# Optimization experiments

Hardware: AMD Instinct MI355X
Metric: run time of the kernel (lower is better)

## Reference

```python
import jax, jax.numpy as jnp
import numpy as np

B, S, D = 1, 2048, 128   # batch, seq_len, num_hidden (== head dim)
H, KVH = 32, 8           # num_heads, num_kv_heads
REP = H // KVH           # num_rep = 4
D_K = 128                # softmax scale denominator sqrt(d_k)
ROPE_THETA = 10000.0


def _rope(x):
    # x: (B, h, S, D). Standard rotate-half RoPE over last dim, positions on axis -2.
    inv_freq = 1.0 / (ROPE_THETA ** (jnp.arange(0, D, 2, dtype=jnp.float32) / D))  # (D/2,)
    ang = jnp.arange(S, dtype=jnp.float32)[:, None] * inv_freq                      # (S, D/2)
    cos = jnp.concatenate([jnp.cos(ang), jnp.cos(ang)], axis=-1)                    # (S, D)
    sin = jnp.concatenate([jnp.sin(ang), jnp.sin(ang)], axis=-1)
    x1, x2 = jnp.split(x, 2, axis=-1)
    rot = jnp.concatenate([-x2, x1], axis=-1)
    return x * cos + rot * sin


def setup_inputs() -> dict:
    key = jax.random.key(0)
    ks = jax.random.split(key, 11)
    w = 0.02
    return {
        "query":  jax.random.normal(ks[0], (B, S, D), jnp.float32),
        "keys":   jax.random.normal(ks[1], (B, S, D), jnp.float32),
        "values": jax.random.normal(ks[2], (B, S, D), jnp.float32),
        "Wq": jax.random.normal(ks[3], (D, H * D), jnp.float32) * w,
        "bq": jnp.zeros((H * D,), jnp.float32),
        "Wk": jax.random.normal(ks[4], (D, KVH * D), jnp.float32) * w,
        "bk": jnp.zeros((KVH * D,), jnp.float32),
        "Wv": jax.random.normal(ks[5], (D, KVH * D), jnp.float32) * w,
        "bv": jnp.zeros((KVH * D,), jnp.float32),
        "Wo": jax.random.normal(ks[6], (H * D, D), jnp.float32) * w,
        "bo": jnp.zeros((D,), jnp.float32),
    }


def reference(query, keys, values, Wq, bq, Wk, bk, Wv, bv, Wo, bo):
    # Projections; faithful to torch .view(): plain reshape (B,S,h*D)->(B,h,S,D), no transpose.
    q = (query @ Wq + bq).reshape(B, H, S, D)
    k = (keys @ Wk + bk).reshape(B, KVH, S, D)
    v = (values @ Wv + bv).reshape(B, KVH, S, D)
    k = _rope(k)
    v = _rope(v)  # module applies RoPE to values too
    # torch repeat tiles kv heads: q head i <-> kv head (i % KVH).
    qg = q.reshape(B, REP, KVH, S, D)
    scores = jnp.einsum('brgsd,bgtd->brgst', qg, k) / jnp.sqrt(jnp.float32(D_K))
    attn = jax.nn.softmax(scores, axis=-1)  # mask=False path, no causal mask
    out = jnp.einsum('brgst,bgtd->brgsd', attn, v).reshape(B, H, S, D)
    out = out.transpose(0, 2, 1, 3).reshape(B, S, H * D)
    return out @ Wo + bo
```

## Files before the change

### kernel.cpp

```cpp
#include <hip/hip_runtime.h>
#include <math.h>


#define SCALE 0.08838834764831843f
#define SCALE_L2E 0.12751878222550723f
#define L2_10K_64 0.20762050593045952f

typedef short bf16x8 __attribute__((ext_vector_type(8)));
typedef float f32x4 __attribute__((ext_vector_type(4)));

__device__ __forceinline__ unsigned short f2b(float f) {
  union { float f; unsigned u; } x; x.f = f;
  return (unsigned short)((x.u + 0x7FFFu + ((x.u >> 16) & 1u)) >> 16);
}
__device__ __forceinline__ float b2f(unsigned short b) {
  union { unsigned u; float f; } x; x.u = ((unsigned)b) << 16;
  return x.f;
}
__device__ __forceinline__ void lds_dma16(void* lds, const void* g) {
  __builtin_amdgcn_global_load_lds(
      (const __attribute__((address_space(1))) unsigned int*)g,
      (__attribute__((address_space(3))) unsigned int*)lds, 16, 0, 0);
}

__global__ __launch_bounds__(256) void prep_weights(
    const float* __restrict__ Wk, const float* __restrict__ Wv,
    const float* __restrict__ Wo, const float* __restrict__ Wq,
    const float* __restrict__ bo,
    unsigned short* __restrict__ Wkt, unsigned short* __restrict__ Wvt,
    unsigned short* __restrict__ Wot, unsigned short* __restrict__ Wq2,
    float* __restrict__ out, int big) {
  __shared__ unsigned short T[64][66];
  int b = blockIdx.x, tid = threadIdx.x;
  const float* W;
  unsigned short* D;
  int K, N, tk, tn;
  if (b < 32) {
    W = Wk; D = Wkt; K = 128; N = 1024; int ti = b;       tk = ti & 1;  tn = ti >> 1;
  } else if (b < 64) {
    W = Wv; D = Wvt; K = 128; N = 1024; int ti = b - 32;  tk = ti & 1;  tn = ti >> 1;
  } else if (b < 192) {
    W = Wo; D = Wot; K = 4096; N = 128; int ti = b - 64;  tk = ti >> 1; tn = ti & 1;
  } else if (b < 320) {
    if (!big) {
      int i0 = ((b - 192) * 256 + tid) * 16;
#pragma unroll
      for (int j = 0; j < 16; ++j) Wq2[i0 + j] = f2b(Wq[i0 + j]);
      return;
    }
    W = Wq; D = Wq2; K = 128; N = 4096; int ti = b - 192; tk = ti & 1;  tn = ti >> 1;
  } else {
    int i0 = ((b - 320) * 256 + tid) * 16;
#pragma unroll
    for (int j = 0; j < 16; ++j) out[i0 + j] = bo[(i0 + j) & 127];
    return;
  }
  int k0 = tk * 64, n0 = tn * 64;
  int c = tid & 63, q = tid >> 6;
#pragma unroll
  for (int i = 0; i < 16; ++i) {
    int r = i * 4 + q;
    T[r][c] = f2b(W[(size_t)(k0 + r) * N + n0 + c]);
  }
  __syncthreads();
#pragma unroll
  for (int i = 0; i < 16; ++i) {
    int r = i * 4 + q;
    D[(size_t)(n0 + r) * K + k0 + c] = T[c][r];
  }
}

__global__ __launch_bounds__(256) void proj_all(
    const float* __restrict__ keys, const float* __restrict__ values,
    const float* __restrict__ query,
    const unsigned short* __restrict__ Wkt, const unsigned short* __restrict__ Wvt,
    const unsigned short* __restrict__ Wqt,
    const float* __restrict__ bk, const float* __restrict__ bv, const float* __restrict__ bq,
    unsigned short* __restrict__ kp, unsigned short* __restrict__ vt,
    unsigned short* __restrict__ qp) {
  int bx = blockIdx.x, m0 = blockIdx.y * 64;
  int tid = threadIdx.x;
  int w = tid >> 6, l = tid & 63;
  int l16 = l & 15, g4 = l >> 4;
  int arow = m0 + w * 16 + l16;
  const f32x4 fz = {0.f, 0.f, 0.f, 0.f};

  if (bx >= 16) {
    int n0 = (bx - 16) * 64;
    f32x4 acc[4];
#pragma unroll
    for (int nb = 0; nb < 4; ++nb) acc[nb] = fz;
#pragma unroll
    for (int kc = 0; kc < 4; ++kc) {
      int kbase = kc * 32 + g4 * 8;
      const float* xp = query + (size_t)arow * 128 + kbase;
      bf16x8 a;
#pragma unroll
      for (int j = 0; j < 8; ++j) a[j] = (short)f2b(xp[j]);
#pragma unroll
      for (int nb = 0; nb < 4; ++nb) {
        bf16x8 b = *(const bf16x8*)(Wqt + (size_t)(n0 + nb * 16 + l16) * 128 + kbase);
        acc[nb] = __builtin_amdgcn_mfma_f32_16x16x32_bf16(a, b, acc[nb], 0, 0, 0);
      }
    }
#pragma unroll
    for (int nb = 0; nb < 4; ++nb) {
      int n = n0 + nb * 16 + l16;
      float bvv = bq[n];
#pragma unroll
      for (int r = 0; r < 4; ++r) {
        int mi = m0 + w * 16 + g4 * 4 + r;
        int h = mi >> 6;
        int s = ((mi & 63) << 5) | (n >> 7);
        qp[((size_t)h * 2048 + s) * 128 + (n & 127)] = f2b(acc[nb][r] + bvv);
      }
    }
    return;
  }

  int vmode = bx >> 3;
  int n0 = (bx & 7) * 128, tb = bx & 7;
  const float* X = vmode ? values : keys;
  const unsigned short* Wt = vmode ? Wvt : Wkt;
  const float* bias = vmode ? bv : bk;
  f32x4 acc[8];
#pragma unroll
  for (int nb = 0; nb < 8; ++nb) acc[nb] = fz;
#pragma unroll
  for (int kc = 0; kc < 4; ++kc) {
    int kbase = kc * 32 + g4 * 8;
    const float* xp = X + (size_t)arow * 128 + kbase;
    bf16x8 a;
#pragma unroll
    for (int j = 0; j < 8; ++j) a[j] = (short)f2b(xp[j]);
#pragma unroll
    for (int nb = 0; nb < 8; ++nb) {
      bf16x8 b = *(const bf16x8*)(Wt + (size_t)(n0 + nb * 16 + l16) * 128 + kbase);
      acc[nb] = __builtin_amdgcn_mfma_f32_16x16x32_bf16(a, b, acc[nb], 0, 0, 0);
    }
  }
#pragma unroll
  for (int nb = 0; nb < 4; ++nb) {
    int d2 = nb * 16 + l16;
    float invf = exp2f(-(float)d2 * L2_10K_64);
    float blo = bias[n0 + d2], bhi = bias[n0 + d2 + 64];
#pragma unroll
    for (int r = 0; r < 4; ++r) {
      int mi = m0 + w * 16 + g4 * 4 + r;
      int t = (mi & 255) * 8 + tb;
      float ang = (float)t * invf;
      float sf, cf;
      __sincosf(ang, &sf, &cf);
      float x1 = acc[nb][r] + blo;
      float x2 = acc[nb + 4][r] + bhi;
      unsigned short lo = f2b(x1 * cf - x2 * sf);
      unsigned short hi = f2b(x2 * cf + x1 * sf);
      int g = mi >> 8;
      if (vmode) {
        vt[(size_t)g * 262144 + (size_t)d2 * 2048 + t] = lo;
        vt[(size_t)g * 262144 + (size_t)(d2 + 64) * 2048 + t] = hi;
      } else {
        kp[(size_t)g * 262144 + (size_t)t * 128 + d2] = lo;
        kp[(size_t)g * 262144 + (size_t)t * 128 + d2 + 64] = hi;
      }
    }
  }
}

__global__ void ws_marker(float* __restrict__ out) {
  out[blockIdx.x * 256 + threadIdx.x] = 12345.0f;
}

template <int FUSED_Q>
__global__ __launch_bounds__(256, 2) void attn_kernel(
    const float* __restrict__ X, const unsigned short* __restrict__ Wqb,
    const float* __restrict__ bq, const unsigned short* __restrict__ qp,
    const unsigned short* __restrict__ kp, const unsigned short* __restrict__ vt,
    const unsigned short* __restrict__ Wot, float* __restrict__ out) {
  __shared__ __align__(16) char smem[59392];
  int bid = blockIdx.x;
  int h = bid & 31, g = h & 7;
  int qi0 = (bid >> 5) * 128;
  int tid = threadIdx.x;
  int w = tid >> 6, l = tid & 63;
  int l16 = l & 15, g4 = l >> 4;

  const f32x4 fz = {0.f, 0.f, 0.f, 0.f};
  bf16x8 qfrag[2][4];

  if (FUSED_Q) {
    unsigned short* Uni = (unsigned short*)smem;
    int r0 = h * 64 + (qi0 >> 5);
    int col0 = tid * 16;
#pragma unroll
    for (int jp = 0; jp < 2; ++jp) {
      float acc[2][16];
#pragma unroll
      for (int j = 0; j < 2; ++j)
#pragma unroll
        for (int cc = 0; cc < 16; ++cc) acc[j][cc] = bq[col0 + cc];
      const float* xr0 = X + (size_t)(r0 + jp * 2) * 128;
      const float* xr1 = xr0 + 128;
      for (int k = 0; k < 128; ++k) {
        float x0 = xr0[k], x1 = xr1[k];
        bf16x8 w0 = *(const bf16x8*)(Wqb + (size_t)k * 4096 + col0);
        bf16x8 w1 = *(const bf16x8*)(Wqb + (size_t)k * 4096 + col0 + 8);
#pragma unroll
        for (int e = 0; e < 8; ++e) {
          float f0 = b2f((unsigned short)w0[e]), f1 = b2f((unsigned short)w1[e]);
          acc[0][e] += x0 * f0; acc[0][8 + e] += x0 * f1;
          acc[1][e] += x1 * f0; acc[1][8 + e] += x1 * f1;
        }
      }
#pragma unroll
      for (int j = 0; j < 2; ++j)
#pragma unroll
        for (int cc = 0; cc < 16; ++cc)
          Uni[(jp * 2 + j) * 4096 + col0 + cc] = f2b(acc[j][cc]);
    }
    __syncthreads();
#pragma unroll
    for (int a = 0; a < 2; ++a) {
      int srow = w * 32 + a * 16 + l16;
      int sj = srow >> 5, scol = (srow & 31) * 128;
#pragma unroll
      for (int kc = 0; kc < 4; ++kc)
        qfrag[a][kc] = *(const bf16x8*)&Uni[sj * 4096 + scol + kc * 32 + g4 * 8];
    }
    __syncthreads();
  } else {
#pragma unroll
    for (int a = 0; a < 2; ++a) {
      const unsigned short* qrow =
          qp + ((size_t)h * 2048 + qi0 + w * 32 + a * 16 + l16) * 128;
#pragma unroll
      for (int kc = 0; kc < 4; ++kc)
        qfrag[a][kc] = *(const bf16x8*)(qrow + kc * 32 + g4 * 8);
    }
  }

  const char* kg = (const char*)(kp + (size_t)g * 262144);
  const char* vg = (const char*)(vt + (size_t)g * 262144);
  unsigned short* PsW = (unsigned short*)(smem + 49152) + w * 1280;

#define STAGE_K(tn, kb)                                                          \
  {                                                                              \
    _Pragma("unroll") for (int i = 0; i < 2; ++i) {                              \
      int off = w * 2048 + i * 1024 + l * 16;                                    \
      int row = off >> 8, ch = (off >> 4) & 15;                                  \
      int rch = ch ^ (row & 7);                                                  \
      lds_dma16(smem + (kb) * 8192 + w * 2048 + i * 1024,                        \
                kg + (size_t)(tn) * 8192 + (size_t)row * 256 + rch * 16);        \
    }                                                                            \
  }
#define STAGE_V(tn, vb)                                                          \
  {                                                                              \
    _Pragma("unroll") for (int i = 0; i < 2; ++i) {                              \
      int off = w * 2048 + i * 1024 + l * 16;                                    \
      int vrow = off >> 6, vcb = off & 63;                                       \
      lds_dma16(smem + 24576 + (vb) * 8192 + w * 2048 + i * 1024,                \
                vg + (size_t)vrow * 4096 + (size_t)(tn) * 64 + vcb);             \
    }                                                                            \
  }

  STAGE_K(0, 0); STAGE_V(0, 0);
  STAGE_K(1, 1); STAGE_V(1, 1);
  __syncthreads();

  f32x4 oacc[2][8];
#pragma unroll
  for (int a = 0; a < 2; ++a)
#pragma unroll
    for (int db = 0; db < 8; ++db) oacc[a][db] = fz;
  float lacc[2][4] = {{0.f, 0.f, 0.f, 0.f}, {0.f, 0.f, 0.f, 0.f}};

  for (int t = 0; t < 64; ++t) {
    int cb = t % 3;
    if (t < 62) {
      int nb3 = (t + 2) % 3;
      STAGE_K(t + 2, nb3);
      STAGE_V(t + 2, nb3);
    }

    f32x4 sacc[2][2];
    sacc[0][0] = fz; sacc[0][1] = fz; sacc[1][0] = fz; sacc[1][1] = fz;
    __builtin_amdgcn_s_setprio(1);
#pragma unroll
    for (int kc = 0; kc < 4; ++kc) {
#pragma unroll
      for (int jb = 0; jb < 2; ++jb) {
        int krow = jb * 16 + l16;
        int rch = (kc * 4 + g4) ^ (krow & 7);
        bf16x8 bfrag = *(const bf16x8*)(smem + cb * 8192 + krow * 256 + rch * 16);
        sacc[0][jb] = __builtin_amdgcn_mfma_f32_16x16x32_bf16(qfrag[0][kc], bfrag, sacc[0][jb], 0, 0, 0);
        sacc[1][jb] = __builtin_amdgcn_mfma_f32_16x16x32_bf16(qfrag[1][kc], bfrag, sacc[1][jb], 0, 0, 0);
      }
    }
    __builtin_amdgcn_s_setprio(0);
#pragma unroll
    for (int a = 0; a < 2; ++a) {
#pragma unroll
      for (int r = 0; r < 4; ++r) {
        unsigned short u0 = f2b(exp2f(sacc[a][0][r] * SCALE_L2E));
        unsigned short u1 = f2b(exp2f(sacc[a][1][r] * SCALE_L2E));
        lacc[a][r] += b2f(u0) + b2f(u1);
        PsW[(a * 16 + g4 * 4 + r) * 40 + l16] = u0;
        PsW[(a * 16 + g4 * 4 + r) * 40 + 16 + l16] = u1;
      }
    }
    bf16x8 pfrag0 = *(const bf16x8*)(PsW + l16 * 40 + g4 * 8);
    bf16x8 pfrag1 = *(const bf16x8*)(PsW + (16 + l16) * 40 + g4 * 8);
    __builtin_amdgcn_s_setprio(1);
#pragma unroll
    for (int db = 0; db < 8; ++db) {
      bf16x8 vfrag = *(const bf16x8*)(smem + 24576 + cb * 8192 + (db * 16 + l16) * 64 + g4 * 16);
      oacc[0][db] = __builtin_amdgcn_mfma_f32_16x16x32_bf16(pfrag0, vfrag, oacc[0][db], 0, 0, 0);
      oacc[1][db] = __builtin_amdgcn_mfma_f32_16x16x32_bf16(pfrag1, vfrag, oacc[1][db], 0, 0, 0);
    }
    __builtin_amdgcn_s_setprio(0);

    if (t < 63) {
      if (t < 62) asm volatile("s_waitcnt vmcnt(4)" ::: "memory");
      else        asm volatile("s_waitcnt vmcnt(0)" ::: "memory");
      __builtin_amdgcn_s_barrier();
      __builtin_amdgcn_sched_barrier(0);
    }
  }

  float invl[2][4];
#pragma unroll
  for (int a = 0; a < 2; ++a)
#pragma unroll
    for (int r = 0; r < 4; ++r) {
      float v = lacc[a][r];
#pragma unroll
      for (int off = 1; off < 16; off <<= 1) v += __shfl_xor(v, off, 64);
      invl[a][r] = 1.f / v;
    }

  __syncthreads();
  unsigned short* Otile = (unsigned short*)smem;
#pragma unroll
  for (int a = 0; a < 2; ++a)
#pragma unroll
    for (int db = 0; db < 8; ++db)
#pragma unroll
      for (int r = 0; r < 4; ++r)
        Otile[(w * 32 + a * 16 + g4 * 4 + r) * 136 + db * 16 + l16] =
            f2b(oacc[a][db][r] * invl[a][r]);
  __syncthreads();
  bf16x8 a2[2][4];
#pragma unroll
  for (int a = 0; a < 2; ++a)
#pragma unroll
    for (int kc = 0; kc < 4; ++kc)
      a2[a][kc] = *(const bf16x8*)&Otile[(w * 32 + a * 16 + l16) * 136 + kc * 32 + g4 * 8];
  f32x4 acc2[2][8];
#pragma unroll
  for (int a = 0; a < 2; ++a)
#pragma unroll
    for (int nb = 0; nb < 8; ++nb) acc2[a][nb] = fz;
#pragma unroll
  for (int kc = 0; kc < 4; ++kc) {
#pragma unroll
    for (int nb = 0; nb < 8; ++nb) {
      bf16x8 b2v = *(const bf16x8*)(Wot + (size_t)(nb * 16 + l16) * 4096 + h * 128 + kc * 32 + g4 * 8);
      acc2[0][nb] = __builtin_amdgcn_mfma_f32_16x16x32_bf16(a2[0][kc], b2v, acc2[0][nb], 0, 0, 0);
      acc2[1][nb] = __builtin_amdgcn_mfma_f32_16x16x32_bf16(a2[1][kc], b2v, acc2[1][nb], 0, 0, 0);
    }
  }
#pragma unroll
  for (int a = 0; a < 2; ++a)
#pragma unroll
    for (int nb = 0; nb < 8; ++nb)
#pragma unroll
      for (int r = 0; r < 4; ++r)
        atomicAdd(&out[(size_t)(qi0 + w * 32 + a * 16 + g4 * 4 + r) * 128 + nb * 16 + l16],
                  acc2[a][nb][r]);
#undef STAGE_K
#undef STAGE_V
}

extern "C" void kernel_launch(void* const* d_in, const int* in_sizes, int n_in,
                              void* d_out, int out_size, void* d_ws, size_t ws_size,
                              hipStream_t stream) {
  const float* query  = (const float*)d_in[0];
  const float* keys   = (const float*)d_in[1];
  const float* values = (const float*)d_in[2];
  const float* Wq = (const float*)d_in[3];
  const float* bq = (const float*)d_in[4];
  const float* Wk = (const float*)d_in[5];
  const float* bk = (const float*)d_in[6];
  const float* Wv = (const float*)d_in[7];
  const float* bv = (const float*)d_in[8];
  const float* Wo = (const float*)d_in[9];
  const float* bo = (const float*)d_in[10];
  float* out = (float*)d_out;
  char* ws = (char*)d_ws;
  const size_t MB = 1024 * 1024;
  if (ws_size < 10 * MB + 512 * 1024) {
    ws_marker<<<1024, 256, 0, stream>>>(out);
    return;
  }
  unsigned short* Wq2   = (unsigned short*)(ws);
  unsigned short* Wkt   = (unsigned short*)(ws + 1 * MB);
  unsigned short* Wvt   = (unsigned short*)(ws + 1 * MB + 256 * 1024);
  unsigned short* Wot   = (unsigned short*)(ws + 1 * MB + 512 * 1024);
  unsigned short* kproj = (unsigned short*)(ws + 2 * MB + 512 * 1024);
  unsigned short* vt    = (unsigned short*)(ws + 6 * MB + 512 * 1024);
  unsigned short* qproj = (unsigned short*)(ws + 10 * MB + 512 * 1024);
  int big = ws_size >= 27 * MB;

  prep_weights<<<384, 256, 0, stream>>>(Wk, Wv, Wo, Wq, bo, Wkt, Wvt, Wot, Wq2, out, big);

  if (big) {
    proj_all<<<dim3(80, 32), 256, 0, stream>>>(keys, values, query, Wkt, Wvt, Wq2,
                                               bk, bv, bq, kproj, vt, qproj);
    attn_kernel<0><<<512, 256, 0, stream>>>(query, Wq2, bq, qproj, kproj, vt, Wot, out);
  } else {
    proj_all<<<dim3(16, 32), 256, 0, stream>>>(keys, values, query, Wkt, Wvt, Wq2,
                                               bk, bv, bq, kproj, vt, qproj);
    attn_kernel<1><<<512, 256, 0, stream>>>(query, Wq2, bq, nullptr, kproj, vt, Wot, out);
  }
}
```

Baseline: 182.2 us.

## Switch attention to 32x32 MFMA with transposed scores and register P redistribution

Result: slower. 338.7 us (+85.9%).

```diff
diff --git a/kernel.cpp b/kernel.cpp
--- a/kernel.cpp
+++ b/kernel.cpp
@@ -2,12 +2,12 @@
 #include <math.h>
 
 
-#define SCALE 0.08838834764831843f
 #define SCALE_L2E 0.12751878222550723f
 #define L2_10K_64 0.20762050593045952f
 
 typedef short bf16x8 __attribute__((ext_vector_type(8)));
 typedef float f32x4 __attribute__((ext_vector_type(4)));
+typedef float f32x16 __attribute__((ext_vector_type(16)));
 
 __device__ __forceinline__ unsigned short f2b(float f) {
   union { float f; unsigned u; } x; x.f = f;
@@ -21,6 +21,21 @@
   __builtin_amdgcn_global_load_lds(
       (const __attribute__((address_space(1))) unsigned int*)g,
       (__attribute__((address_space(3))) unsigned int*)lds, 16, 0, 0);
+}
+__device__ __forceinline__ unsigned cvtpk(float lo, float hi) {
+  unsigned r;
+  asm("v_cvt_pk_bf16_f32 %0, %1, %2" : "=v"(r) : "v"(lo), "v"(hi));
+  return r;
+}
+#define PLSWAP(a, b) asm("v_permlane32_swap_b32 %0, %1" : "+v"(a), "+v"(b))
+
+__device__ __forceinline__ void redist(unsigned pw[8], bf16x8* f0, bf16x8* f1) {
+  PLSWAP(pw[0], pw[2]); PLSWAP(pw[1], pw[3]);
+  PLSWAP(pw[4], pw[6]); PLSWAP(pw[5], pw[7]);
+  union { unsigned u[4]; bf16x8 v; } a, b;
+  a.u[0] = pw[0]; a.u[1] = pw[1]; a.u[2] = pw[2]; a.u[3] = pw[3];
+  b.u[0] = pw[4]; b.u[1] = pw[5]; b.u[2] = pw[6]; b.u[3] = pw[7];
+  *f0 = a.v; *f1 = b.v;
 }
 
 __global__ __launch_bounds__(256) void prep_weights(
@@ -177,16 +192,16 @@
     const float* __restrict__ bq, const unsigned short* __restrict__ qp,
     const unsigned short* __restrict__ kp, const unsigned short* __restrict__ vt,
     const unsigned short* __restrict__ Wot, float* __restrict__ out) {
-  __shared__ __align__(16) char smem[59392];
+  __shared__ __align__(16) char smem[65536];
   int bid = blockIdx.x;
   int h = bid & 31, g = h & 7;
   int qi0 = (bid >> 5) * 128;
   int tid = threadIdx.x;
   int w = tid >> 6, l = tid & 63;
-  int l16 = l & 15, g4 = l >> 4;
-
-  const f32x4 fz = {0.f, 0.f, 0.f, 0.f};
-  bf16x8 qfrag[2][4];
+  int l31 = l & 31, hi = l >> 5;
+
+  const f32x16 fz16 = {0.f};
+  bf16x8 qfrag[8];
 
   if (FUSED_Q) {
     unsigned short* Uni = (unsigned short*)smem;
@@ -219,164 +234,130 @@
           Uni[(jp * 2 + j) * 4096 + col0 + cc] = f2b(acc[j][cc]);
     }
     __syncthreads();
-#pragma unroll
-    for (int a = 0; a < 2; ++a) {
-      int srow = w * 32 + a * 16 + l16;
-      int sj = srow >> 5, scol = (srow & 31) * 128;
-#pragma unroll
-      for (int kc = 0; kc < 4; ++kc)
-        qfrag[a][kc] = *(const bf16x8*)&Uni[sj * 4096 + scol + kc * 32 + g4 * 8];
-    }
+    int srow = w * 32 + l31;
+    int sj = srow >> 5, scol = (srow & 31) * 128;
+#pragma unroll
+    for (int kc = 0; kc < 8; ++kc)
+      qfrag[kc] = *(const bf16x8*)&Uni[sj * 4096 + scol + kc * 16 + hi * 8];
     __syncthreads();
   } else {
-#pragma unroll
-    for (int a = 0; a < 2; ++a) {
-      const unsigned short* qrow =
-          qp + ((size_t)h * 2048 + qi0 + w * 32 + a * 16 + l16) * 128;
-#pragma unroll
-      for (int kc = 0; kc < 4; ++kc)
-        qfrag[a][kc] = *(const bf16x8*)(qrow + kc * 32 + g4 * 8);
-    }
+    const unsigned short* qrow = qp + ((size_t)h * 2048 + qi0 + w * 32 + l31) * 128;
+#pragma unroll
+    for (int kc = 0; kc < 8; ++kc)
+      qfrag[kc] = *(const bf16x8*)(qrow + kc * 16 + hi * 8);
   }
 
   const char* kg = (const char*)(kp + (size_t)g * 262144);
   const char* vg = (const char*)(vt + (size_t)g * 262144);
-  unsigned short* PsW = (unsigned short*)(smem + 49152) + w * 1280;
-
-#define STAGE_K(tn, kb)                                                          \
-  {                                                                              \
-    _Pragma("unroll") for (int i = 0; i < 2; ++i) {                              \
-      int off = w * 2048 + i * 1024 + l * 16;                                    \
-      int row = off >> 8, ch = (off >> 4) & 15;                                  \
-      int rch = ch ^ (row & 7);                                                  \
-      lds_dma16(smem + (kb) * 8192 + w * 2048 + i * 1024,                        \
-                kg + (size_t)(tn) * 8192 + (size_t)row * 256 + rch * 16);        \
-    }                                                                            \
-  }
-#define STAGE_V(tn, vb)                                                          \
-  {                                                                              \
-    _Pragma("unroll") for (int i = 0; i < 2; ++i) {                              \
-      int off = w * 2048 + i * 1024 + l * 16;                                    \
-      int vrow = off >> 6, vcb = off & 63;                                       \
-      lds_dma16(smem + 24576 + (vb) * 8192 + w * 2048 + i * 1024,                \
-                vg + (size_t)vrow * 4096 + (size_t)(tn) * 64 + vcb);             \
-    }                                                                            \
-  }
-
-  STAGE_K(0, 0); STAGE_V(0, 0);
-  STAGE_K(1, 1); STAGE_V(1, 1);
+
+#define STAGE_K(tn, kb)                                                         \
+  {                                                                             \
+    _Pragma("unroll") for (int i = 0; i < 4; ++i) {                             \
+      int off = w * 4096 + i * 1024 + l * 16;                                   \
+      int row = off >> 8, ch = (off >> 4) & 15;                                 \
+      int rch = ch ^ (row & 15);                                                \
+      lds_dma16(smem + (kb) * 16384 + w * 4096 + i * 1024,                      \
+                kg + (size_t)(tn) * 16384 + (size_t)row * 256 + rch * 16);      \
+    }                                                                           \
+  }
+#define STAGE_V(tn, vb)                                                         \
+  {                                                                             \
+    _Pragma("unroll") for (int i = 0; i < 4; ++i) {                             \
+      int off = w * 4096 + i * 1024 + l * 16;                                   \
+      int row = off >> 7, ch = (off >> 4) & 7;                                  \
+      int rch = ch ^ (row & 7);                                                 \
+      lds_dma16(smem + 32768 + (vb) * 16384 + w * 4096 + i * 1024,              \
+                vg + (size_t)row * 4096 + (size_t)(tn) * 128 + rch * 16);       \
+    }                                                                           \
+  }
+
+  STAGE_K(0, 0);
+  STAGE_V(0, 0);
   __syncthreads();
 
-  f32x4 oacc[2][8];
-#pragma unroll
-  for (int a = 0; a < 2; ++a)
-#pragma unroll
-    for (int db = 0; db < 8; ++db) oacc[a][db] = fz;
-  float lacc[2][4] = {{0.f, 0.f, 0.f, 0.f}, {0.f, 0.f, 0.f, 0.f}};
-
-  for (int t = 0; t < 64; ++t) {
-    int cb = t % 3;
-    if (t < 62) {
-      int nb3 = (t + 2) % 3;
-      STAGE_K(t + 2, nb3);
-      STAGE_V(t + 2, nb3);
-    }
-
-    f32x4 sacc[2][2];
-    sacc[0][0] = fz; sacc[0][1] = fz; sacc[1][0] = fz; sacc[1][1] = fz;
-    __builtin_amdgcn_s_setprio(1);
-#pragma unroll
-    for (int kc = 0; kc < 4; ++kc) {
-#pragma unroll
-      for (int jb = 0; jb < 2; ++jb) {
-        int krow = jb * 16 + l16;
-        int rch = (kc * 4 + g4) ^ (krow & 7);
-        bf16x8 bfrag = *(const bf16x8*)(smem + cb * 8192 + krow * 256 + rch * 16);
-        sacc[0][jb] = __builtin_amdgcn_mfma_f32_16x16x32_bf16(qfrag[0][kc], bfrag, sacc[0][jb], 0, 0, 0);
-        sacc[1][jb] = __builtin_amdgcn_mfma_f32_16x16x32_bf16(qfrag[1][kc], bfrag, sacc[1][jb], 0, 0, 0);
-      }
-    }
-    __builtin_amdgcn_s_setprio(0);
-#pragma unroll
-    for (int a = 0; a < 2; ++a) {
-#pragma unroll
-      for (int r = 0; r < 4; ++r) {
-        unsigned short u0 = f2b(exp2f(sacc[a][0][r] * SCALE_L2E));
-        unsigned short u1 = f2b(exp2f(sacc[a][1][r] * SCALE_L2E));
-        lacc[a][r] += b2f(u0) + b2f(u1);
-        PsW[(a * 16 + g4 * 4 + r) * 40 + l16] = u0;
-        PsW[(a * 16 + g4 * 4 + r) * 40 + 16 + l16] = u1;
-      }
-    }
-    bf16x8 pfrag0 = *(const bf16x8*)(PsW + l16 * 40 + g4 * 8);
-    bf16x8 pfrag1 = *(const bf16x8*)(PsW + (16 + l16) * 40 + g4 * 8);
-    __builtin_amdgcn_s_setprio(1);
-#pragma unroll
-    for (int db = 0; db < 8; ++db) {
-      bf16x8 vfrag = *(const bf16x8*)(smem + 24576 + cb * 8192 + (db * 16 + l16) * 64 + g4 * 16);
-      oacc[0][db] = __builtin_amdgcn_mfma_f32_16x16x32_bf16(pfrag0, vfrag, oacc[0][db], 0, 0, 0);
-      oacc[1][db] = __builtin_amdgcn_mfma_f32_16x16x32_bf16(pfrag1, vfrag, oacc[1][db], 0, 0, 0);
-    }
-    __builtin_amdgcn_s_setprio(0);
-
-    if (t < 63) {
-      if (t < 62) asm volatile("s_waitcnt vmcnt(4)" ::: "memory");
-      else        asm volatile("s_waitcnt vmcnt(0)" ::: "memory");
-      __builtin_amdgcn_s_barrier();
-      __builtin_amdgcn_sched_barrier(0);
-    }
-  }
-
-  float invl[2][4];
-#pragma unroll
-  for (int a = 0; a < 2; ++a)
-#pragma unroll
-    for (int r = 0; r < 4; ++r) {
-      float v = lacc[a][r];
-#pragma unroll
-      for (int off = 1; off < 16; off <<= 1) v += __shfl_xor(v, off, 64);
-      invl[a][r] = 1.f / v;
-    }
-
-  __syncthreads();
-  unsigned short* Otile = (unsigned short*)smem;
-#pragma unroll
-  for (int a = 0; a < 2; ++a)
-#pragma unroll
-    for (int db = 0; db < 8; ++db)
-#pragma unroll
-      for (int r = 0; r < 4; ++r)
-        Otile[(w * 32 + a * 16 + g4 * 4 + r) * 136 + db * 16 + l16] =
-            f2b(oacc[a][db][r] * invl[a][r]);
-  __syncthreads();
-  bf16x8 a2[2][4];
-#pragma unroll
-  for (int a = 0; a < 2; ++a)
-#pragma unroll
-    for (int kc = 0; kc < 4; ++kc)
-      a2[a][kc] = *(const bf16x8*)&Otile[(w * 32 + a * 16 + l16) * 136 + kc * 32 + g4 * 8];
-  f32x4 acc2[2][8];
-#pragma unroll
-  for (int a = 0; a < 2; ++a)
-#pragma unroll
-    for (int nb = 0; nb < 8; ++nb) acc2[a][nb] = fz;
-#pragma unroll
-  for (int kc = 0; kc < 4; ++kc) {
-#pragma unroll
-    for (int nb = 0; nb < 8; ++nb) {
-      bf16x8 b2v = *(const bf16x8*)(Wot + (size_t)(nb * 16 + l16) * 4096 + h * 128 + kc * 32 + g4 * 8);
-      acc2[0][nb] = __builtin_amdgcn_mfma_f32_16x16x32_bf16(a2[0][kc], b2v, acc2[0][nb], 0, 0, 0);
-      acc2[1][nb] = __builtin_amdgcn_mfma_f32_16x16x32_bf16(a2[1][kc], b2v, acc2[1][nb], 0, 0, 0);
-    }
-  }
-#pragma unroll
-  for (int a = 0; a < 2; ++a)
-#pragma unroll
-    for (int nb = 0; nb < 8; ++nb)
-#pragma unroll
-      for (int r = 0; r < 4; ++r)
-        atomicAdd(&out[(size_t)(qi0 + w * 32 + a * 16 + g4 * 4 + r) * 128 + nb * 16 + l16],
-                  acc2[a][nb][r]);
+  f32x16 oacc[4];
+#pragma unroll
+  for (int db = 0; db < 4; ++db) oacc[db] = fz16;
+  float lacc = 0.f;
+
+  int c = 0;
+  for (int t = 0; t < 32; ++t) {
+    if (t < 31) { STAGE_K(t + 1, c ^ 1); STAGE_V(t + 1, c ^ 1); }
+
+#pragma unroll
+    for (int jb = 0; jb < 2; ++jb) {
+      f32x16 sacc = fz16;
+      __builtin_amdgcn_s_setprio(1);
+#pragma unroll
+      for (int kc = 0; kc < 8; ++kc) {
+        int row = jb * 32 + l31;
+        int rch = (kc * 2 + hi) ^ (row & 15);
+        bf16x8 kfrag = *(const bf16x8*)(smem + c * 16384 + row * 256 + rch * 16);
+        sacc = __builtin_amdgcn_mfma_f32_32x32x16_bf16(kfrag, qfrag[kc], sacc, 0, 0, 0);
+      }
+      __builtin_amdgcn_s_setprio(0);
+      float p[16];
+#pragma unroll
+      for (int j = 0; j < 16; ++j) {
+        p[j] = exp2f(sacc[j] * SCALE_L2E);
+        lacc += p[j];
+      }
+      unsigned pw[8];
+#pragma unroll
+      for (int m = 0; m < 8; ++m) pw[m] = cvtpk(p[2 * m], p[2 * m + 1]);
+      bf16x8 pf0, pf1;
+      redist(pw, &pf0, &pf1);
+      __builtin_amdgcn_s_setprio(1);
+#pragma unroll
+      for (int ks = 0; ks < 2; ++ks) {
+        int ksg = jb * 2 + ks;
+        bf16x8 pf = ks ? pf1 : pf0;
+#pragma unroll
+        for (int db = 0; db < 4; ++db) {
+          int row = db * 32 + l31;
+          int rch = (ksg * 2 + hi) ^ (row & 7);
+          bf16x8 vfrag = *(const bf16x8*)(smem + 32768 + c * 16384 + row * 128 + rch * 16);
+          oacc[db] = __builtin_amdgcn_mfma_f32_32x32x16_bf16(vfrag, pf, oacc[db], 0, 0, 0);
+        }
+      }
+      __builtin_amdgcn_s_setprio(0);
+    }
+    __syncthreads();
+    c ^= 1;
+  }
+
+  float ltot = lacc + __shfl_xor(lacc, 32, 64);
+  float invl = 1.f / ltot;
+
+  f32x16 acc2[4];
+#pragma unroll
+  for (int nb = 0; nb < 4; ++nb) acc2[nb] = fz16;
+  bf16x8 ofrag[8];
+#pragma unroll
+  for (int db = 0; db < 4; ++db) {
+    unsigned pw[8];
+#pragma unroll
+    for (int m = 0; m < 8; ++m)
+      pw[m] = cvtpk(oacc[db][2 * m] * invl, oacc[db][2 * m + 1] * invl);
+    redist(pw, &ofrag[db * 2], &ofrag[db * 2 + 1]);
+  }
+#pragma unroll
+  for (int ks = 0; ks < 8; ++ks) {
+#pragma unroll
+    for (int nb = 0; nb < 4; ++nb) {
+      bf16x8 wof = *(const bf16x8*)(Wot + (size_t)(nb * 32 + l31) * 4096 + h * 128 + ks * 16 + hi * 8);
+      acc2[nb] = __builtin_amdgcn_mfma_f32_32x32x16_bf16(wof, ofrag[ks], acc2[nb], 0, 0, 0);
+    }
+  }
+  size_t qrow = (size_t)(qi0 + w * 32 + l31);
+#pragma unroll
+  for (int nb = 0; nb < 4; ++nb) {
+#pragma unroll
+    for (int j = 0; j < 16; ++j) {
+      int no = nb * 32 + (j & 3) + 8 * (j >> 2) + 4 * hi;
+      atomicAdd(&out[qrow * 128 + no], acc2[nb][j]);
+    }
+  }
 #undef STAGE_K
 #undef STAGE_V
 }
```
